# Performance work log

Hardware: AMD Instinct MI355X
Metric: run time of the kernel (lower is better)

The kernel has to match this reference:

```python
import jax, jax.numpy as jnp
import numpy as np
import math

B, TSRC, TTGT, DM, DI, H = 2, 2048, 2048, 1024, 1024, 16
DH = DI // H
LN_EPS = 1e-5


def setup_inputs() -> dict:
    key = jax.random.key(0)
    ks = iter(jax.random.split(key, 40))
    def p(*shape):
        return jax.random.normal(next(ks), shape, jnp.float32) * 0.02
    inp = {
        "enc_out_vecs": jax.random.normal(next(ks), (B, TSRC, DM), jnp.float32),
        "output_vecs": jax.random.normal(next(ks), (B, TTGT, DM), jnp.float32),
    }
    for tag in ("dd", "ed"):
        inp["Wq_" + tag] = p(DM, DI); inp["bq_" + tag] = jnp.zeros((DI,), jnp.float32)
        inp["Wk_" + tag] = p(DM, DI); inp["bk_" + tag] = jnp.zeros((DI,), jnp.float32)
        inp["Wv_" + tag] = p(DM, DI); inp["bv_" + tag] = jnp.zeros((DI,), jnp.float32)
        inp["Wo_" + tag] = p(DI, DM); inp["bo_" + tag] = jnp.zeros((DM,), jnp.float32)
        inp["W1_" + tag] = p(DM, 2 * DM); inp["b1_" + tag] = jnp.zeros((2 * DM,), jnp.float32)
        inp["W2_" + tag] = p(2 * DM, DM); inp["b2_" + tag] = jnp.zeros((DM,), jnp.float32)
        inp["g1_" + tag] = jnp.ones((DM,), jnp.float32); inp["be1_" + tag] = jnp.zeros((DM,), jnp.float32)
        inp["g2_" + tag] = jnp.ones((DM,), jnp.float32); inp["be2_" + tag] = jnp.zeros((DM,), jnp.float32)
    return inp


def _ln(x, g, b):
    m = jnp.mean(x, axis=-1, keepdims=True)
    v = jnp.var(x, axis=-1, keepdims=True)
    return (x - m) * jax.lax.rsqrt(v + LN_EPS) * g + b


def _mha(xq, xkv, Wq, bq, Wk, bk, Wv, bv, causal):
    Bb, Tq, _ = xq.shape
    Tk = xkv.shape[1]
    q = (xq @ Wq + bq).reshape(Bb, Tq, H, DH)
    k = (xkv @ Wk + bk).reshape(Bb, Tk, H, DH)
    v = (xkv @ Wv + bv).reshape(Bb, Tk, H, DH)
    s = jnp.einsum("bqhd,bkhd->bhqk", q, k) / math.sqrt(DH)
    if causal:
        mask = jnp.where(jnp.arange(Tk)[None, :] > jnp.arange(Tq)[:, None], -jnp.inf, 0.0)
        s = s + mask
    w = jax.nn.softmax(s, axis=-1)
    return jnp.einsum("bhqk,bkhd->bqhd", w, v).reshape(Bb, Tq, H * DH)


def reference(enc_out_vecs, output_vecs,
              Wq_dd, bq_dd, Wk_dd, bk_dd, Wv_dd, bv_dd, Wo_dd, bo_dd,
              W1_dd, b1_dd, W2_dd, b2_dd, g1_dd, be1_dd, g2_dd, be2_dd,
              Wq_ed, bq_ed, Wk_ed, bk_ed, Wv_ed, bv_ed, Wo_ed, bo_ed,
              W1_ed, b1_ed, W2_ed, b2_ed, g1_ed, be1_ed, g2_ed, be2_ed):
    # masked self-attention over decoder inputs
    x = output_vecs
    a = _mha(x, x, Wq_dd, bq_dd, Wk_dd, bk_dd, Wv_dd, bv_dd, causal=True)
    x = _ln(a @ Wo_dd + bo_dd + x, g1_dd, be1_dd)
    x = _ln(x + jax.nn.relu(x @ W1_dd + b1_dd) @ W2_dd + b2_dd, g2_dd, be2_dd)
    # cross attention against encoder outputs
    a = _mha(x, enc_out_vecs, Wq_ed, bq_ed, Wk_ed, bk_ed, Wv_ed, bv_ed, causal=False)
    x = _ln(a @ Wo_ed + bo_ed + x, g1_ed, be1_ed)
    x = _ln(jax.nn.relu(x @ W1_ed + b1_ed) @ W2_ed + b2_ed + x, g2_ed, be2_ed)
    return x
```

## Files before the change

kernel.cpp:

```cpp
#include <hip/hip_runtime.h>
#include <stdint.h>

#define DEV __device__ __forceinline__
typedef unsigned short u16;
typedef __attribute__((ext_vector_type(8))) short bf16x8;
typedef __attribute__((ext_vector_type(4))) float f32x4;

#define WAITVM0 asm volatile("s_waitcnt vmcnt(0)" ::: "memory")
#define QSCALE 0.18033688011112042f

DEV u16 f2bf(float f) {
  union { float f; uint32_t u; } x; x.f = f;
  uint32_t r = x.u + 0x7fffu + ((x.u >> 16) & 1u);
  return (u16)(r >> 16);
}

DEV uint32_t cvt_pk_bf16(float a, float b) {
  uint32_t r;
  asm("v_cvt_pk_bf16_f32 %0, %1, %2" : "=v"(r) : "v"(a), "v"(b));
  return r;
}

__global__ __launch_bounds__(256) void k_cvt_bf16(const float* __restrict__ in,
                                                  u16* __restrict__ out, int n4) {
  int i = blockIdx.x * blockDim.x + threadIdx.x;
  if (i >= n4) return;
  float4 v = reinterpret_cast<const float4*>(in)[i];
  ushort4 o = make_ushort4(f2bf(v.x), f2bf(v.y), f2bf(v.z), f2bf(v.w));
  reinterpret_cast<ushort4*>(out)[i] = o;
}

struct WTJob { const float* W; u16* WT; int K, M, msh, start; };
struct WTJobs { WTJob j[12]; };

__global__ void k_wT_all(WTJobs jobs) {
  __shared__ float tile[32][33];
  int b = blockIdx.x;
  int i = 0;
#pragma unroll
  for (int t = 1; t < 12; ++t)
    if (b >= jobs.j[t].start) i = t;
  const WTJob J = jobs.j[i];
  int rel = b - J.start;
  int m0 = (rel & ((1 << J.msh) - 1)) << 5;
  int k0 = (rel >> J.msh) << 5;
  int tx = threadIdx.x, ty = threadIdx.y;
#pragma unroll
  for (int q = 0; q < 4; ++q)
    tile[ty + q * 8][tx] = J.W[(size_t)(k0 + ty + q * 8) * J.M + m0 + tx];
  __syncthreads();
#pragma unroll
  for (int q = 0; q < 4; ++q)
    J.WT[(size_t)(m0 + ty + q * 8) * J.K + k0 + tx] = f2bf(tile[tx][ty + q * 8]);
}

template<int R>
DEV void stage_tile(const u16* __restrict__ g, int strideElems, u16* lds, int tid, int wv) {
#pragma unroll
  for (int t = 0; t < R / 32; ++t) {
    int idx = t * 256 + tid;
    int row = idx >> 3;
    int b = (idx & 7) << 4;
    int sb = b ^ ((row & 7) << 4);
    const char* src = (const char*)g + (size_t)row * strideElems * 2 + sb;
    char* dst = (char*)lds + (size_t)(t * 256 + wv * 64) * 16;
    __builtin_amdgcn_global_load_lds((const __attribute__((address_space(1))) void*)src,
                                     (__attribute__((address_space(3))) void*)dst, 16, 0, 0);
  }
}

DEV bf16x8 lds_frag(const u16* lds, int row, int kel) {
  int off = row * 128 + ((kel * 2) ^ ((row & 7) << 4));
  return *(const bf16x8*)((const char*)lds + off);
}

template<int JT, int MODE>
__global__ __launch_bounds__(256) void k_gemm(const u16* __restrict__ A, int lda,
                                              const u16* __restrict__ BT,
                                              const float* __restrict__ bias,
                                              void* __restrict__ C, int ldc, int K) {
  constexpr int BN = JT * 32;
  __shared__ __align__(16) u16 A_lds[2][128 * 64];
  __shared__ __align__(16) u16 B_lds[2][BN * 64];
  const int tid = threadIdx.x, lane = tid & 63, wv = tid >> 6;
  const int wm = wv >> 1, wn = wv & 1;
  const int bm0 = blockIdx.y * 128, bn0 = blockIdx.x * BN;
  const int lr = lane & 15, lk = (lane >> 4) * 8, r0 = (lane >> 4) * 4;

  f32x4 acc[4][JT];
#pragma unroll
  for (int i = 0; i < 4; ++i)
#pragma unroll
    for (int j = 0; j < JT; ++j) acc[i][j] = f32x4{0.f, 0.f, 0.f, 0.f};

  stage_tile<128>(A + (size_t)bm0 * lda, lda, A_lds[0], tid, wv);
  stage_tile<BN>(BT + (size_t)bn0 * K, K, B_lds[0], tid, wv);
  WAITVM0;
  __builtin_amdgcn_s_barrier();

  int cur = 0;
  for (int k0 = 0; k0 < K; k0 += 64) {
    if (k0 + 64 < K) {
      stage_tile<128>(A + (size_t)bm0 * lda + k0 + 64, lda, A_lds[cur ^ 1], tid, wv);
      stage_tile<BN>(BT + (size_t)bn0 * K + k0 + 64, K, B_lds[cur ^ 1], tid, wv);
    }
#pragma unroll
    for (int kk = 0; kk < 2; ++kk) {
      bf16x8 af[4], bfr[JT];
#pragma unroll
      for (int i = 0; i < 4; ++i) af[i] = lds_frag(A_lds[cur], wm * 64 + i * 16 + lr, kk * 32 + lk);
#pragma unroll
      for (int j = 0; j < JT; ++j) bfr[j] = lds_frag(B_lds[cur], wn * (JT * 16) + j * 16 + lr, kk * 32 + lk);
#pragma unroll
      for (int i = 0; i < 4; ++i)
#pragma unroll
        for (int j = 0; j < JT; ++j)
          acc[i][j] = __builtin_amdgcn_mfma_f32_16x16x32_bf16(af[i], bfr[j], acc[i][j], 0, 0, 0);
    }
    WAITVM0;
    __builtin_amdgcn_s_barrier();
    cur ^= 1;
  }

#pragma unroll
  for (int j = 0; j < JT; ++j) {
    int col = bn0 + wn * (JT * 16) + j * 16 + lr;
    float bv = bias[col];
#pragma unroll
    for (int i = 0; i < 4; ++i) {
      int rowb = bm0 + wm * 64 + i * 16 + r0;
      if constexpr (MODE == 0) {
#pragma unroll
        for (int r = 0; r < 4; ++r)
          ((float*)C)[(size_t)(rowb + r) * ldc + col] = acc[i][j][r] + bv;
      } else {
#pragma unroll
        for (int r = 0; r < 4; ++r) {
          float v = acc[i][j][r] + bv;
          if constexpr (MODE == 2) v = fmaxf(v, 0.f);
          ((u16*)C)[(size_t)(rowb + r) * ldc + col] = f2bf(v);
        }
      }
    }
  }
}

__global__ __launch_bounds__(256) void k_qkv(const u16* __restrict__ Aq, const u16* __restrict__ Akv,
                                             const u16* __restrict__ BT,
                                             const float* __restrict__ bq, const float* __restrict__ bk,
                                             const float* __restrict__ bv,
                                             u16* __restrict__ Qb, u16* __restrict__ Kb,
                                             u16* __restrict__ Vt, int K) {
  __shared__ __align__(16) u16 A_lds[2][128 * 64];
  __shared__ __align__(16) u16 B_lds[2][64 * 64];
  const int tid = threadIdx.x, lane = tid & 63, wv = tid >> 6;
  const int wm = wv >> 1, wn = wv & 1;
  const int bm0 = blockIdx.y * 128, bn0 = blockIdx.x * 64;
  const int seg = bn0 >> 10;
  const u16* A = (seg == 0) ? Aq : Akv;
  const int lr = lane & 15, lk = (lane >> 4) * 8, r0 = (lane >> 4) * 4;

  f32x4 acc[4][2];
#pragma unroll
  for (int i = 0; i < 4; ++i)
#pragma unroll
    for (int j = 0; j < 2; ++j) acc[i][j] = f32x4{0.f, 0.f, 0.f, 0.f};

  stage_tile<128>(A + (size_t)bm0 * K, K, A_lds[0], tid, wv);
  stage_tile<64>(BT + (size_t)bn0 * K, K, B_lds[0], tid, wv);
  WAITVM0;
  __builtin_amdgcn_s_barrier();

  int cur = 0;
  for (int k0 = 0; k0 < K; k0 += 64) {
    if (k0 + 64 < K) {
      stage_tile<128>(A + (size_t)bm0 * K + k0 + 64, K, A_lds[cur ^ 1], tid, wv);
      stage_tile<64>(BT + (size_t)bn0 * K + k0 + 64, K, B_lds[cur ^ 1], tid, wv);
    }
#pragma unroll
    for (int kk = 0; kk < 2; ++kk) {
      bf16x8 af[4], bfr[2];
#pragma unroll
      for (int i = 0; i < 4; ++i) af[i] = lds_frag(A_lds[cur], wm * 64 + i * 16 + lr, kk * 32 + lk);
#pragma unroll
      for (int j = 0; j < 2; ++j) bfr[j] = lds_frag(B_lds[cur], wn * 32 + j * 16 + lr, kk * 32 + lk);
#pragma unroll
      for (int i = 0; i < 4; ++i)
#pragma unroll
        for (int j = 0; j < 2; ++j)
          acc[i][j] = __builtin_amdgcn_mfma_f32_16x16x32_bf16(af[i], bfr[j], acc[i][j], 0, 0, 0);
    }
    WAITVM0;
    __builtin_amdgcn_s_barrier();
    cur ^= 1;
  }

#pragma unroll
  for (int j = 0; j < 2; ++j) {
    int col = bn0 + wn * 32 + j * 16 + lr;
    int cl = col & 1023;
#pragma unroll
    for (int i = 0; i < 4; ++i) {
      int rowb = bm0 + wm * 64 + i * 16 + r0;
      if (seg == 0) {
        float bb = bq[cl];
#pragma unroll
        for (int r = 0; r < 4; ++r)
          Qb[(size_t)(rowb + r) * 1024 + cl] = f2bf((acc[i][j][r] + bb) * QSCALE);
      } else if (seg == 1) {
        float bb = bk[cl];
#pragma unroll
        for (int r = 0; r < 4; ++r)
          Kb[(size_t)(rowb + r) * 1024 + cl] = f2bf(acc[i][j][r] + bb);
      } else {
        float bb = bv[cl];
        int bidx = rowb >> 11, t = rowb & 2047;
        ushort4 o = make_ushort4(f2bf(acc[i][j][0] + bb), f2bf(acc[i][j][1] + bb),
                                 f2bf(acc[i][j][2] + bb), f2bf(acc[i][j][3] + bb));
        *reinterpret_cast<ushort4*>(&Vt[((size_t)bidx * 1024 + cl) * 2048 + t]) = o;
      }
    }
  }
}

__global__ __launch_bounds__(256) void k_ln(const float* __restrict__ Rm, const float* __restrict__ X,
                                            const float* __restrict__ g, const float* __restrict__ be,
                                            float* __restrict__ Y, u16* __restrict__ Yb) {
  int row = blockIdx.x;
  size_t base4 = (size_t)row * 256;
  int t = threadIdx.x;
  float4 a = reinterpret_cast<const float4*>(Rm)[base4 + t];
  float4 x = reinterpret_cast<const float4*>(X)[base4 + t];
  float v0 = a.x + x.x, v1 = a.y + x.y, v2 = a.z + x.z, v3 = a.w + x.w;
  float s = v0 + v1 + v2 + v3;
  float ss = v0 * v0 + v1 * v1 + v2 * v2 + v3 * v3;
#pragma unroll
  for (int m = 1; m < 64; m <<= 1) { s += __shfl_xor(s, m); ss += __shfl_xor(ss, m); }
  __shared__ float red[8];
  int wv = t >> 6;
  if ((t & 63) == 0) { red[wv] = s; red[4 + wv] = ss; }
  __syncthreads();
  s = red[0] + red[1] + red[2] + red[3];
  ss = red[4] + red[5] + red[6] + red[7];
  float mean = s * (1.f / 1024.f);
  float var = ss * (1.f / 1024.f) - mean * mean;
  float rstd = rsqrtf(var + 1e-5f);
  float4 gv = reinterpret_cast<const float4*>(g)[t];
  float4 bv = reinterpret_cast<const float4*>(be)[t];
  float o0 = (v0 - mean) * rstd * gv.x + bv.x;
  float o1 = (v1 - mean) * rstd * gv.y + bv.y;
  float o2 = (v2 - mean) * rstd * gv.z + bv.z;
  float o3 = (v3 - mean) * rstd * gv.w + bv.w;
  reinterpret_cast<float4*>(Y)[base4 + t] = make_float4(o0, o1, o2, o3);
  if (Yb) {
    ushort4 ob = make_ushort4(f2bf(o0), f2bf(o1), f2bf(o2), f2bf(o3));
    reinterpret_cast<ushort4*>(Yb)[base4 + t] = ob;
  }
}

template<bool CAUSAL>
__global__ __launch_bounds__(256) void k_attn(const u16* __restrict__ Q, const u16* __restrict__ Kg,
                                              const u16* __restrict__ Vt, u16* __restrict__ O, int T) {
  __shared__ __align__(16) u16 K_lds[2][64 * 64];
  __shared__ __align__(16) u16 V_lds[2][64 * 64];
  __shared__ __align__(16) u16 p_lds[4][16 * 64];
  const int tid = threadIdx.x, lane = tid & 63, wv = tid >> 6;
  const int h = blockIdx.y, b = blockIdx.z;
  const int qx = CAUSAL ? (gridDim.x - 1 - blockIdx.x) : blockIdx.x;
  const int q0 = qx * 64;
  const int qw = q0 + wv * 16;
  const int lq = lane & 15, g = lane >> 4, lk = g * 8;
  const int swz = (lq & 7) << 4;
  const size_t qkbase = ((size_t)b * T) * 1024 + h * 64;
  const size_t vbase = ((size_t)b * 1024 + h * 64) * T;

  bf16x8 aq[2];
#pragma unroll
  for (int kk = 0; kk < 2; ++kk)
    aq[kk] = *reinterpret_cast<const bf16x8*>(
        &Q[qkbase + (size_t)(qw + lq) * 1024 + kk * 32 + lk]);

  f32x4 acc[4];
#pragma unroll
  for (int j = 0; j < 4; ++j) acc[j] = f32x4{0.f, 0.f, 0.f, 0.f};
  float lsum = 0.f;

  const int nt = CAUSAL ? (qx + 1) : (T >> 6);

  stage_tile<64>(Kg + qkbase, 1024, K_lds[0], tid, wv);
  stage_tile<64>(Vt + vbase, T, V_lds[0], tid, wv);
  WAITVM0;
  __builtin_amdgcn_s_barrier();

  char* pw = (char*)p_lds[wv];
  int cur = 0;
  for (int it = 0; it < nt; ++it) {
    const int kv0 = it << 6;
    if (it + 1 < nt) {
      stage_tile<64>(Kg + qkbase + (size_t)(kv0 + 64) * 1024, 1024, K_lds[cur ^ 1], tid, wv);
      stage_tile<64>(Vt + vbase + kv0 + 64, T, V_lds[cur ^ 1], tid, wv);
    }
    f32x4 st[4];
    __builtin_amdgcn_s_setprio(1);
#pragma unroll
    for (int j = 0; j < 4; ++j) {
      bf16x8 bk0 = lds_frag(K_lds[cur], j * 16 + lq, lk);
      bf16x8 bk1 = lds_frag(K_lds[cur], j * 16 + lq, 32 + lk);
      f32x4 t0 = f32x4{0.f, 0.f, 0.f, 0.f};
      t0 = __builtin_amdgcn_mfma_f32_16x16x32_bf16(bk0, aq[0], t0, 0, 0, 0);
      t0 = __builtin_amdgcn_mfma_f32_16x16x32_bf16(bk1, aq[1], t0, 0, 0, 0);
      st[j] = t0;
    }
    __builtin_amdgcn_s_setprio(0);
    uint32_t pk[8];
    if (CAUSAL && it == nt - 1) {
      const int qrow = qw + lq;
#pragma unroll
      for (int j = 0; j < 4; ++j) {
        float p[4];
#pragma unroll
        for (int r = 0; r < 4; ++r) {
          float e = __builtin_exp2f(st[j][r]);
          int kv = kv0 + j * 16 + g * 4 + r;
          e = (kv > qrow) ? 0.f : e;
          p[r] = e;
          lsum += e;
        }
        pk[2 * j] = cvt_pk_bf16(p[0], p[1]);
        pk[2 * j + 1] = cvt_pk_bf16(p[2], p[3]);
      }
    } else {
#pragma unroll
      for (int j = 0; j < 4; ++j) {
        float p[4];
#pragma unroll
        for (int r = 0; r < 4; ++r) {
          float e = __builtin_exp2f(st[j][r]);
          p[r] = e;
          lsum += e;
        }
        pk[2 * j] = cvt_pk_bf16(p[0], p[1]);
        pk[2 * j + 1] = cvt_pk_bf16(p[2], p[3]);
      }
    }
#pragma unroll
    for (int j = 0; j < 4; ++j)
      *reinterpret_cast<uint2*>(pw + lq * 128 + ((j * 32 + g * 8) ^ swz)) =
          make_uint2(pk[2 * j], pk[2 * j + 1]);
    bf16x8 pf0 = *reinterpret_cast<const bf16x8*>(pw + lq * 128 + ((g * 16) ^ swz));
    bf16x8 pf1 = *reinterpret_cast<const bf16x8*>(pw + lq * 128 + ((g * 16 + 64) ^ swz));
    __builtin_amdgcn_s_setprio(1);
#pragma unroll
    for (int j2 = 0; j2 < 4; ++j2) {
      bf16x8 v0 = lds_frag(V_lds[cur], j2 * 16 + lq, lk);
      bf16x8 v1 = lds_frag(V_lds[cur], j2 * 16 + lq, 32 + lk);
      acc[j2] = __builtin_amdgcn_mfma_f32_16x16x32_bf16(v0, pf0, acc[j2], 0, 0, 0);
      acc[j2] = __builtin_amdgcn_mfma_f32_16x16x32_bf16(v1, pf1, acc[j2], 0, 0, 0);
    }
    __builtin_amdgcn_s_setprio(0);
    WAITVM0;
    __builtin_amdgcn_s_barrier();
    cur ^= 1;
  }

  lsum += __shfl_xor(lsum, 16);
  lsum += __shfl_xor(lsum, 32);
  float inv = 1.f / lsum;
  size_t rb = qkbase + (size_t)(qw + lq) * 1024;
#pragma unroll
  for (int j2 = 0; j2 < 4; ++j2) {
    ushort4 o = make_ushort4(f2bf(acc[j2][0] * inv), f2bf(acc[j2][1] * inv),
                             f2bf(acc[j2][2] * inv), f2bf(acc[j2][3] * inv));
    *reinterpret_cast<ushort4*>(&O[rb + j2 * 16 + g * 4]) = o;
  }
}

extern "C" void kernel_launch(void* const* d_in, const int* in_sizes, int n_in,
                              void* d_out, int out_size, void* d_ws, size_t ws_size,
                              hipStream_t stream) {
  const int T = 2048;
  const float* enc = (const float*)d_in[0];
  const float* outv = (const float*)d_in[1];
  auto F = [&](int i) { return (const float*)d_in[i]; };

  size_t off = 0;
  auto alloc = [&](size_t bytes) {
    void* p = (char*)d_ws + off;
    off += (bytes + 255) & ~(size_t)255;
    return p;
  };

  const int tdK[12] = {1024, 1024, 1024, 1024, 1024, 2048, 1024, 1024, 1024, 1024, 1024, 2048};
  const int tdM[12] = {1024, 1024, 1024, 1024, 2048, 1024, 1024, 1024, 1024, 1024, 2048, 1024};
  const int tdIdx[12] = {2, 4, 6, 8, 10, 12, 18, 20, 22, 24, 26, 28};
  u16* WT_[12];
  for (int i = 0; i < 12; ++i) WT_[i] = (u16*)alloc((size_t)tdK[i] * tdM[i] * 2);

  u16* Xb0 = (u16*)alloc(4096ull * 1024 * 2);
  u16* Eb = (u16*)alloc(4096ull * 1024 * 2);
  u16* Qb = (u16*)alloc(4096ull * 1024 * 2);
  u16* Kb = (u16*)alloc(4096ull * 1024 * 2);
  u16* Vt = (u16*)alloc(4096ull * 1024 * 2);
  u16* Ab = (u16*)alloc(4096ull * 1024 * 2);
  u16* Hb = (u16*)alloc(4096ull * 2048 * 2);
  u16* Xbc = (u16*)alloc(4096ull * 1024 * 2);
  float* Rf = (float*)alloc(4096ull * 1024 * 4);
  float* Xfa = (float*)alloc(4096ull * 1024 * 4);
  float* Xfb = (float*)alloc(4096ull * 1024 * 4);

  k_cvt_bf16<<<4096, 256, 0, stream>>>(outv, Xb0, 4096 * 1024 / 4);
  k_cvt_bf16<<<4096, 256, 0, stream>>>(enc, Eb, 4096 * 1024 / 4);

  WTJobs jobs;
  int start = 0;
  for (int i = 0; i < 12; ++i) {
    int msh = (tdM[i] == 2048) ? 6 : 5;
    jobs.j[i] = {F(tdIdx[i]), WT_[i], tdK[i], tdM[i], msh, start};
    start += (tdM[i] >> 5) * (tdK[i] >> 5);
  }
  k_wT_all<<<start, dim3(32, 8), 0, stream>>>(jobs);

  dim3 gq(48, 32);
  dim3 g64(16, 32);
  dim3 g128(16, 32);
  dim3 ga(32, 16, 2);

  k_qkv<<<gq, 256, 0, stream>>>(Xb0, Xb0, WT_[0], F(3), F(5), F(7), Qb, Kb, Vt, 1024);
  k_attn<true><<<ga, 256, 0, stream>>>(Qb, Kb, Vt, Ab, T);
  k_gemm<2, 0><<<g64, 256, 0, stream>>>(Ab, 1024, WT_[3], F(9), Rf, 1024, 1024);
  k_ln<<<4096, 256, 0, stream>>>(Rf, outv, F(14), F(15), Xfa, Xbc);
  k_gemm<4, 2><<<g128, 256, 0, stream>>>(Xbc, 1024, WT_[4], F(11), Hb, 2048, 1024);
  k_gemm<2, 0><<<g64, 256, 0, stream>>>(Hb, 2048, WT_[5], F(13), Rf, 1024, 2048);
  k_ln<<<4096, 256, 0, stream>>>(Rf, Xfa, F(16), F(17), Xfb, Xbc);

  k_qkv<<<gq, 256, 0, stream>>>(Xbc, Eb, WT_[6], F(19), F(21), F(23), Qb, Kb, Vt, 1024);
  k_attn<false><<<ga, 256, 0, stream>>>(Qb, Kb, Vt, Ab, T);
  k_gemm<2, 0><<<g64, 256, 0, stream>>>(Ab, 1024, WT_[9], F(25), Rf, 1024, 1024);
  k_ln<<<4096, 256, 0, stream>>>(Rf, Xfb, F(30), F(31), Xfa, Xbc);
  k_gemm<4, 2><<<g128, 256, 0, stream>>>(Xbc, 1024, WT_[10], F(27), Hb, 2048, 1024);
  k_gemm<2, 0><<<g64, 256, 0, stream>>>(Hb, 2048, WT_[11], F(29), Rf, 1024, 2048);
  k_ln<<<4096, 256, 0, stream>>>(Rf, Xfa, F(32), F(33), (float*)d_out, (u16*)nullptr);
}
```

Measured before the change: 446.9 us.

## Use 128x128 GEMM tiles everywhere, merge input casts, streamline attention staging

All GEMMs and the QKV projection now use 128x128 output tiles with 4x4 MFMA accumulators per wave instead of 128x64 tiles. This raises data reuse per block but halves the grid for the N=1024 GEMMs, leaving 256 blocks. The two fp32-to-bf16 input conversions are merged into one launch. The attention kernel precomputes swizzled fragment offsets and advances K/V staging pointers incrementally to cut per-iteration address arithmetic.

```diff
diff --git a/kernel.cpp b/kernel.cpp
--- a/kernel.cpp
+++ b/kernel.cpp
@@ -6,6 +6,8 @@
 typedef __attribute__((ext_vector_type(8))) short bf16x8;
 typedef __attribute__((ext_vector_type(4))) float f32x4;
 
+#define AS1 __attribute__((address_space(1)))
+#define AS3 __attribute__((address_space(3)))
 #define WAITVM0 asm volatile("s_waitcnt vmcnt(0)" ::: "memory")
 #define QSCALE 0.18033688011112042f
 
@@ -21,13 +23,16 @@
   return r;
 }
 
-__global__ __launch_bounds__(256) void k_cvt_bf16(const float* __restrict__ in,
-                                                  u16* __restrict__ out, int n4) {
+__global__ __launch_bounds__(256) void k_cvt2(const float* __restrict__ a, const float* __restrict__ bsrc,
+                                              u16* __restrict__ oa, u16* __restrict__ ob, int n4) {
   int i = blockIdx.x * blockDim.x + threadIdx.x;
-  if (i >= n4) return;
-  float4 v = reinterpret_cast<const float4*>(in)[i];
-  ushort4 o = make_ushort4(f2bf(v.x), f2bf(v.y), f2bf(v.z), f2bf(v.w));
-  reinterpret_cast<ushort4*>(out)[i] = o;
+  const float* s;
+  u16* o;
+  int k;
+  if (i < n4) { s = a; o = oa; k = i; }
+  else        { s = bsrc; o = ob; k = i - n4; }
+  float4 v = reinterpret_cast<const float4*>(s)[k];
+  reinterpret_cast<ushort4*>(o)[k] = make_ushort4(f2bf(v.x), f2bf(v.y), f2bf(v.z), f2bf(v.w));
 }
 
 struct WTJob { const float* W; u16* WT; int K, M, msh, start; };
@@ -64,8 +69,7 @@
     int sb = b ^ ((row & 7) << 4);
     const char* src = (const char*)g + (size_t)row * strideElems * 2 + sb;
     char* dst = (char*)lds + (size_t)(t * 256 + wv * 64) * 16;
-    __builtin_amdgcn_global_load_lds((const __attribute__((address_space(1))) void*)src,
-                                     (__attribute__((address_space(3))) void*)dst, 16, 0, 0);
+    __builtin_amdgcn_global_load_lds((const AS1 void*)src, (AS3 void*)dst, 16, 0, 0);
   }
 }
 
@@ -74,27 +78,26 @@
   return *(const bf16x8*)((const char*)lds + off);
 }
 
-template<int JT, int MODE>
+template<int MODE>
 __global__ __launch_bounds__(256) void k_gemm(const u16* __restrict__ A, int lda,
                                               const u16* __restrict__ BT,
                                               const float* __restrict__ bias,
                                               void* __restrict__ C, int ldc, int K) {
-  constexpr int BN = JT * 32;
   __shared__ __align__(16) u16 A_lds[2][128 * 64];
-  __shared__ __align__(16) u16 B_lds[2][BN * 64];
+  __shared__ __align__(16) u16 B_lds[2][128 * 64];
   const int tid = threadIdx.x, lane = tid & 63, wv = tid >> 6;
   const int wm = wv >> 1, wn = wv & 1;
-  const int bm0 = blockIdx.y * 128, bn0 = blockIdx.x * BN;
+  const int bm0 = blockIdx.y * 128, bn0 = blockIdx.x * 128;
   const int lr = lane & 15, lk = (lane >> 4) * 8, r0 = (lane >> 4) * 4;
 
-  f32x4 acc[4][JT];
+  f32x4 acc[4][4];
 #pragma unroll
   for (int i = 0; i < 4; ++i)
 #pragma unroll
-    for (int j = 0; j < JT; ++j) acc[i][j] = f32x4{0.f, 0.f, 0.f, 0.f};
+    for (int j = 0; j < 4; ++j) acc[i][j] = f32x4{0.f, 0.f, 0.f, 0.f};
 
   stage_tile<128>(A + (size_t)bm0 * lda, lda, A_lds[0], tid, wv);
-  stage_tile<BN>(BT + (size_t)bn0 * K, K, B_lds[0], tid, wv);
+  stage_tile<128>(BT + (size_t)bn0 * K, K, B_lds[0], tid, wv);
   WAITVM0;
   __builtin_amdgcn_s_barrier();
 
@@ -102,19 +105,19 @@
   for (int k0 = 0; k0 < K; k0 += 64) {
     if (k0 + 64 < K) {
       stage_tile<128>(A + (size_t)bm0 * lda + k0 + 64, lda, A_lds[cur ^ 1], tid, wv);
-      stage_tile<BN>(BT + (size_t)bn0 * K + k0 + 64, K, B_lds[cur ^ 1], tid, wv);
+      stage_tile<128>(BT + (size_t)bn0 * K + k0 + 64, K, B_lds[cur ^ 1], tid, wv);
     }
 #pragma unroll
     for (int kk = 0; kk < 2; ++kk) {
-      bf16x8 af[4], bfr[JT];
+      bf16x8 af[4], bfr[4];
 #pragma unroll
       for (int i = 0; i < 4; ++i) af[i] = lds_frag(A_lds[cur], wm * 64 + i * 16 + lr, kk * 32 + lk);
 #pragma unroll
-      for (int j = 0; j < JT; ++j) bfr[j] = lds_frag(B_lds[cur], wn * (JT * 16) + j * 16 + lr, kk * 32 + lk);
+      for (int j = 0; j < 4; ++j) bfr[j] = lds_frag(B_lds[cur], wn * 64 + j * 16 + lr, kk * 32 + lk);
 #pragma unroll
       for (int i = 0; i < 4; ++i)
 #pragma unroll
-        for (int j = 0; j < JT; ++j)
+        for (int j = 0; j < 4; ++j)
           acc[i][j] = __builtin_amdgcn_mfma_f32_16x16x32_bf16(af[i], bfr[j], acc[i][j], 0, 0, 0);
     }
     WAITVM0;
@@ -123,8 +126,8 @@
   }
 
 #pragma unroll
-  for (int j = 0; j < JT; ++j) {
-    int col = bn0 + wn * (JT * 16) + j * 16 + lr;
+  for (int j = 0; j < 4; ++j) {
+    int col = bn0 + wn * 64 + j * 16 + lr;
     float bv = bias[col];
 #pragma unroll
     for (int i = 0; i < 4; ++i) {
@@ -136,8 +139,7 @@
       } else {
 #pragma unroll
         for (int r = 0; r < 4; ++r) {
-          float v = acc[i][j][r] + bv;
-          if constexpr (MODE == 2) v = fmaxf(v, 0.f);
+          float v = fmaxf(acc[i][j][r] + bv, 0.f);
           ((u16*)C)[(size_t)(rowb + r) * ldc + col] = f2bf(v);
         }
       }
@@ -152,22 +154,22 @@
                                              u16* __restrict__ Qb, u16* __restrict__ Kb,
                                              u16* __restrict__ Vt, int K) {
   __shared__ __align__(16) u16 A_lds[2][128 * 64];
-  __shared__ __align__(16) u16 B_lds[2][64 * 64];
+  __shared__ __align__(16) u16 B_lds[2][128 * 64];
   const int tid = threadIdx.x, lane = tid & 63, wv = tid >> 6;
   const int wm = wv >> 1, wn = wv & 1;
-  const int bm0 = blockIdx.y * 128, bn0 = blockIdx.x * 64;
+  const int bm0 = blockIdx.y * 128, bn0 = blockIdx.x * 128;
   const int seg = bn0 >> 10;
   const u16* A = (seg == 0) ? Aq : Akv;
   const int lr = lane & 15, lk = (lane >> 4) * 8, r0 = (lane >> 4) * 4;
 
-  f32x4 acc[4][2];
+  f32x4 acc[4][4];
 #pragma unroll
   for (int i = 0; i < 4; ++i)
 #pragma unroll
-    for (int j = 0; j < 2; ++j) acc[i][j] = f32x4{0.f, 0.f, 0.f, 0.f};
+    for (int j = 0; j < 4; ++j) acc[i][j] = f32x4{0.f, 0.f, 0.f, 0.f};
 
   stage_tile<128>(A + (size_t)bm0 * K, K, A_lds[0], tid, wv);
-  stage_tile<64>(BT + (size_t)bn0 * K, K, B_lds[0], tid, wv);
+  stage_tile<128>(BT + (size_t)bn0 * K, K, B_lds[0], tid, wv);
   WAITVM0;
   __builtin_amdgcn_s_barrier();
 
@@ -175,19 +177,19 @@
   for (int k0 = 0; k0 < K; k0 += 64) {
     if (k0 + 64 < K) {
       stage_tile<128>(A + (size_t)bm0 * K + k0 + 64, K, A_lds[cur ^ 1], tid, wv);
-      stage_tile<64>(BT + (size_t)bn0 * K + k0 + 64, K, B_lds[cur ^ 1], tid, wv);
+      stage_tile<128>(BT + (size_t)bn0 * K + k0 + 64, K, B_lds[cur ^ 1], tid, wv);
     }
 #pragma unroll
     for (int kk = 0; kk < 2; ++kk) {
-      bf16x8 af[4], bfr[2];
+      bf16x8 af[4], bfr[4];
 #pragma unroll
       for (int i = 0; i < 4; ++i) af[i] = lds_frag(A_lds[cur], wm * 64 + i * 16 + lr, kk * 32 + lk);
 #pragma unroll
-      for (int j = 0; j < 2; ++j) bfr[j] = lds_frag(B_lds[cur], wn * 32 + j * 16 + lr, kk * 32 + lk);
+      for (int j = 0; j < 4; ++j) bfr[j] = lds_frag(B_lds[cur], wn * 64 + j * 16 + lr, kk * 32 + lk);
 #pragma unroll
       for (int i = 0; i < 4; ++i)
 #pragma unroll
-        for (int j = 0; j < 2; ++j)
+        for (int j = 0; j < 4; ++j)
           acc[i][j] = __builtin_amdgcn_mfma_f32_16x16x32_bf16(af[i], bfr[j], acc[i][j], 0, 0, 0);
     }
     WAITVM0;
@@ -196,8 +198,8 @@
   }
 
 #pragma unroll
-  for (int j = 0; j < 2; ++j) {
-    int col = bn0 + wn * 32 + j * 16 + lr;
+  for (int j = 0; j < 4; ++j) {
+    int col = bn0 + wn * 64 + j * 16 + lr;
     int cl = col & 1023;
 #pragma unroll
     for (int i = 0; i < 4; ++i) {
@@ -269,16 +271,35 @@
   const int qx = CAUSAL ? (gridDim.x - 1 - blockIdx.x) : blockIdx.x;
   const int q0 = qx * 64;
   const int qw = q0 + wv * 16;
-  const int lq = lane & 15, g = lane >> 4, lk = g * 8;
+  const int lq = lane & 15, g = lane >> 4;
   const int swz = (lq & 7) << 4;
+  const int fb0 = lq * 128 + ((g * 16) ^ swz);
+  const int fb1 = lq * 128 + ((g * 16 + 64) ^ swz);
   const size_t qkbase = ((size_t)b * T) * 1024 + h * 64;
   const size_t vbase = ((size_t)b * 1024 + h * 64) * T;
 
-  bf16x8 aq[2];
-#pragma unroll
-  for (int kk = 0; kk < 2; ++kk)
-    aq[kk] = *reinterpret_cast<const bf16x8*>(
-        &Q[qkbase + (size_t)(qw + lq) * 1024 + kk * 32 + lk]);
+  bf16x8 aq0, aq1;
+  {
+    const u16* qp = Q + qkbase + (size_t)(qw + lq) * 1024 + g * 8;
+    aq0 = *reinterpret_cast<const bf16x8*>(qp);
+    aq1 = *reinterpret_cast<const bf16x8*>(qp + 32);
+  }
+
+  const int srow = tid >> 3;
+  const int ssb = ((tid & 7) << 4) ^ ((srow & 7) << 4);
+  const char* ksrc = (const char*)(Kg + qkbase) + (size_t)srow * 2048 + ssb;
+  const char* vsrc = (const char*)(Vt + vbase) + (size_t)srow * ((size_t)T * 2) + ssb;
+  const int vstep2 = T * 64;
+  const uint32_t doff = (uint32_t)((tid & 192) << 4);
+
+  auto stage = [&](const char* kp, const char* vp, int buf) {
+    char* kd = (char*)K_lds[buf] + doff;
+    char* vd = (char*)V_lds[buf] + doff;
+    __builtin_amdgcn_global_load_lds((const AS1 void*)kp, (AS3 void*)kd, 16, 0, 0);
+    __builtin_amdgcn_global_load_lds((const AS1 void*)(kp + 65536), (AS3 void*)(kd + 4096), 16, 0, 0);
+    __builtin_amdgcn_global_load_lds((const AS1 void*)vp, (AS3 void*)vd, 16, 0, 0);
+    __builtin_amdgcn_global_load_lds((const AS1 void*)(vp + vstep2), (AS3 void*)(vd + 4096), 16, 0, 0);
+  };
 
   f32x4 acc[4];
 #pragma unroll
@@ -287,28 +308,32 @@
 
   const int nt = CAUSAL ? (qx + 1) : (T >> 6);
 
-  stage_tile<64>(Kg + qkbase, 1024, K_lds[0], tid, wv);
-  stage_tile<64>(Vt + vbase, T, V_lds[0], tid, wv);
+  stage(ksrc, vsrc, 0);
   WAITVM0;
   __builtin_amdgcn_s_barrier();
+  ksrc += 131072;
+  vsrc += 128;
 
   char* pw = (char*)p_lds[wv];
   int cur = 0;
   for (int it = 0; it < nt; ++it) {
     const int kv0 = it << 6;
     if (it + 1 < nt) {
-      stage_tile<64>(Kg + qkbase + (size_t)(kv0 + 64) * 1024, 1024, K_lds[cur ^ 1], tid, wv);
-      stage_tile<64>(Vt + vbase + kv0 + 64, T, V_lds[cur ^ 1], tid, wv);
-    }
+      stage(ksrc, vsrc, cur ^ 1);
+      ksrc += 131072;
+      vsrc += 128;
+    }
+    const char* kb = (const char*)K_lds[cur];
+    const char* vb = (const char*)V_lds[cur];
     f32x4 st[4];
     __builtin_amdgcn_s_setprio(1);
 #pragma unroll
     for (int j = 0; j < 4; ++j) {
-      bf16x8 bk0 = lds_frag(K_lds[cur], j * 16 + lq, lk);
-      bf16x8 bk1 = lds_frag(K_lds[cur], j * 16 + lq, 32 + lk);
+      bf16x8 bk0 = *reinterpret_cast<const bf16x8*>(kb + fb0 + j * 2048);
+      bf16x8 bk1 = *reinterpret_cast<const bf16x8*>(kb + fb1 + j * 2048);
       f32x4 t0 = f32x4{0.f, 0.f, 0.f, 0.f};
-      t0 = __builtin_amdgcn_mfma_f32_16x16x32_bf16(bk0, aq[0], t0, 0, 0, 0);
-      t0 = __builtin_amdgcn_mfma_f32_16x16x32_bf16(bk1, aq[1], t0, 0, 0, 0);
+      t0 = __builtin_amdgcn_mfma_f32_16x16x32_bf16(bk0, aq0, t0, 0, 0, 0);
+      t0 = __builtin_amdgcn_mfma_f32_16x16x32_bf16(bk1, aq1, t0, 0, 0, 0);
       st[j] = t0;
     }
     __builtin_amdgcn_s_setprio(0);
@@ -317,43 +342,42 @@
       const int qrow = qw + lq;
 #pragma unroll
       for (int j = 0; j < 4; ++j) {
-        float p[4];
-#pragma unroll
-        for (int r = 0; r < 4; ++r) {
-          float e = __builtin_exp2f(st[j][r]);
-          int kv = kv0 + j * 16 + g * 4 + r;
-          e = (kv > qrow) ? 0.f : e;
-          p[r] = e;
-          lsum += e;
-        }
-        pk[2 * j] = cvt_pk_bf16(p[0], p[1]);
-        pk[2 * j + 1] = cvt_pk_bf16(p[2], p[3]);
+        float p0 = __builtin_exp2f(st[j][0]);
+        float p1 = __builtin_exp2f(st[j][1]);
+        float p2 = __builtin_exp2f(st[j][2]);
+        float p3 = __builtin_exp2f(st[j][3]);
+        int kvb = kv0 + j * 16 + g * 4;
+        p0 = (kvb > qrow) ? 0.f : p0;
+        p1 = (kvb + 1 > qrow) ? 0.f : p1;
+        p2 = (kvb + 2 > qrow) ? 0.f : p2;
+        p3 = (kvb + 3 > qrow) ? 0.f : p3;
+        lsum += (p0 + p1) + (p2 + p3);
+        pk[2 * j] = cvt_pk_bf16(p0, p1);
+        pk[2 * j + 1] = cvt_pk_bf16(p2, p3);
       }
     } else {
 #pragma unroll
       for (int j = 0; j < 4; ++j) {
-        float p[4];
-#pragma unroll
-        for (int r = 0; r < 4; ++r) {
-          float e = __builtin_exp2f(st[j][r]);
-          p[r] = e;
-          lsum += e;
-        }
-        pk[2 * j] = cvt_pk_bf16(p[0], p[1]);
-        pk[2 * j + 1] = cvt_pk_bf16(p[2], p[3]);
+        float p0 = __builtin_exp2f(st[j][0]);
+        float p1 = __builtin_exp2f(st[j][1]);
+        float p2 = __builtin_exp2f(st[j][2]);
+        float p3 = __builtin_exp2f(st[j][3]);
+        lsum += (p0 + p1) + (p2 + p3);
+        pk[2 * j] = cvt_pk_bf16(p0, p1);
+        pk[2 * j + 1] = cvt_pk_bf16(p2, p3);
       }
     }
 #pragma unroll
     for (int j = 0; j < 4; ++j)
       *reinterpret_cast<uint2*>(pw + lq * 128 + ((j * 32 + g * 8) ^ swz)) =
           make_uint2(pk[2 * j], pk[2 * j + 1]);
-    bf16x8 pf0 = *reinterpret_cast<const bf16x8*>(pw + lq * 128 + ((g * 16) ^ swz));
-    bf16x8 pf1 = *reinterpret_cast<const bf16x8*>(pw + lq * 128 + ((g * 16 + 64) ^ swz));
+    bf16x8 pf0 = *reinterpret_cast<const bf16x8*>(pw + fb0);
+    bf16x8 pf1 = *reinterpret_cast<const bf16x8*>(pw + fb1);
     __builtin_amdgcn_s_setprio(1);
 #pragma unroll
     for (int j2 = 0; j2 < 4; ++j2) {
-      bf16x8 v0 = lds_frag(V_lds[cur], j2 * 16 + lq, lk);
-      bf16x8 v1 = lds_frag(V_lds[cur], j2 * 16 + lq, 32 + lk);
+      bf16x8 v0 = *reinterpret_cast<const bf16x8*>(vb + fb0 + j2 * 2048);
+      bf16x8 v1 = *reinterpret_cast<const bf16x8*>(vb + fb1 + j2 * 2048);
       acc[j2] = __builtin_amdgcn_mfma_f32_16x16x32_bf16(v0, pf0, acc[j2], 0, 0, 0);
       acc[j2] = __builtin_amdgcn_mfma_f32_16x16x32_bf16(v1, pf1, acc[j2], 0, 0, 0);
     }
@@ -408,8 +432,7 @@
   float* Xfa = (float*)alloc(4096ull * 1024 * 4);
   float* Xfb = (float*)alloc(4096ull * 1024 * 4);
 
-  k_cvt_bf16<<<4096, 256, 0, stream>>>(outv, Xb0, 4096 * 1024 / 4);
-  k_cvt_bf16<<<4096, 256, 0, stream>>>(enc, Eb, 4096 * 1024 / 4);
+  k_cvt2<<<8192, 256, 0, stream>>>(outv, enc, Xb0, Eb, 4096 * 1024 / 4);
 
   WTJobs jobs;
   int start = 0;
@@ -420,24 +443,24 @@
   }
   k_wT_all<<<start, dim3(32, 8), 0, stream>>>(jobs);
 
-  dim3 gq(48, 32);
-  dim3 g64(16, 32);
-  dim3 g128(16, 32);
+  dim3 gq(24, 32);
+  dim3 g1k(8, 32);
+  dim3 g2k(16, 32);
   dim3 ga(32, 16, 2);
 
   k_qkv<<<gq, 256, 0, stream>>>(Xb0, Xb0, WT_[0], F(3), F(5), F(7), Qb, Kb, Vt, 1024);
   k_attn<true><<<ga, 256, 0, stream>>>(Qb, Kb, Vt, Ab, T);
-  k_gemm<2, 0><<<g64, 256, 0, stream>>>(Ab, 1024, WT_[3], F(9), Rf, 1024, 1024);
+  k_gemm<0><<<g1k, 256, 0, stream>>>(Ab, 1024, WT_[3], F(9), Rf, 1024, 1024);
   k_ln<<<4096, 256, 0, stream>>>(Rf, outv, F(14), F(15), Xfa, Xbc);
-  k_gemm<4, 2><<<g128, 256, 0, stream>>>(Xbc, 1024, WT_[4], F(11), Hb, 2048, 1024);
-  k_gemm<2, 0><<<g64, 256, 0, stream>>>(Hb, 2048, WT_[5], F(13), Rf, 1024, 2048);
+  k_gemm<2><<<g2k, 256, 0, stream>>>(Xbc, 1024, WT_[4], F(11), Hb, 2048, 1024);
+  k_gemm<0><<<g1k, 256, 0, stream>>>(Hb, 2048, WT_[5], F(13), Rf, 1024, 2048);
   k_ln<<<4096, 256, 0, stream>>>(Rf, Xfa, F(16), F(17), Xfb, Xbc);
 
   k_qkv<<<gq, 256, 0, stream>>>(Xbc, Eb, WT_[6], F(19), F(21), F(23), Qb, Kb, Vt, 1024);
   k_attn<false><<<ga, 256, 0, stream>>>(Qb, Kb, Vt, Ab, T);
-  k_gemm<2, 0><<<g64, 256, 0, stream>>>(Ab, 1024, WT_[9], F(25), Rf, 1024, 1024);
+  k_gemm<0><<<g1k, 256, 0, stream>>>(Ab, 1024, WT_[9], F(25), Rf, 1024, 1024);
   k_ln<<<4096, 256, 0, stream>>>(Rf, Xfb, F(30), F(31), Xfa, Xbc);
-  k_gemm<4, 2><<<g128, 256, 0, stream>>>(Xbc, 1024, WT_[10], F(27), Hb, 2048, 1024);
-  k_gemm<2, 0><<<g64, 256, 0, stream>>>(Hb, 2048, WT_[11], F(29), Rf, 1024, 2048);
+  k_gemm<2><<<g2k, 256, 0, stream>>>(Xbc, 1024, WT_[10], F(27), Hb, 2048, 1024);
+  k_gemm<0><<<g1k, 256, 0, stream>>>(Hb, 2048, WT_[11], F(29), Rf, 1024, 2048);
   k_ln<<<4096, 256, 0, stream>>>(Rf, Xfa, F(32), F(33), (float*)d_out, (u16*)nullptr);
 }
```

Measured after the change: 486.1 us. 1.09x slower.
